# Performance work log

Measured on AMD Instinct MI355X. Metric: run time of the kernel, lower is better.

Reference implementation:

```python
import jax, jax.numpy as jnp
import numpy as np

B, T, N, F, E, L = 2, 2, 10000, 128, 160000, 2


def setup_inputs() -> dict:
    key = jax.random.key(0)
    k = jax.random.split(key, 6)
    feature = jax.random.normal(k[0], (B, T, N, F), jnp.float32)
    edge_src = jax.random.randint(k[1], (E,), 0, N, jnp.int32)
    edge_dst = jax.random.randint(k[2], (E,), 0, N, jnp.int32)
    s = 1.0 / np.sqrt(F).astype(np.float32)
    W_self = jax.random.normal(k[3], (L, F, F), jnp.float32) * s
    W_neigh = jax.random.normal(k[4], (L, F, F), jnp.float32) * s
    b = jnp.zeros((L, F), jnp.float32)
    return dict(feature=feature, W_self=W_self, W_neigh=W_neigh, b=b,
                edge_src=edge_src, edge_dst=edge_dst)


def reference(feature, W_self, W_neigh, b, edge_src, edge_dst):
    # feature: [B, T, N, Fin]; edge (src -> dst) as in dgl.from_scipy(csr).
    Bs, Ts, Ns, Fin = feature.shape
    num_layers = W_self.shape[0]
    # in-degree per dst node; mean over zero in-degree nodes is 0 (DGL semantics)
    deg = jax.ops.segment_sum(jnp.ones(edge_dst.shape, jnp.float32), edge_dst,
                              num_segments=Ns)
    inv_deg = jnp.where(deg > 0, 1.0 / jnp.maximum(deg, 1.0), 0.0)  # [N]
    # node-major layout for gather/scatter: [N, B, T, F]
    h = jnp.transpose(feature, (2, 0, 1, 3))
    for l in range(num_layers):
        msg = h[edge_src]  # [E, B, T, F] irregular gather
        agg = jax.ops.segment_sum(msg, edge_dst, num_segments=Ns)
        h_neigh = agg * inv_deg[:, None, None, None]  # mean aggregation
        h = (jnp.einsum('nbtf,fg->nbtg', h, W_self[l])
             + jnp.einsum('nbtf,fg->nbtg', h_neigh, W_neigh[l])
             + b[l])
    # res.permute(0,2,1,3) in torch -> [B, T, N, Fout]
    return jnp.transpose(h, (1, 2, 0, 3))
```

## Files before the change

### kernel.cpp

```cpp
#include <hip/hip_runtime.h>

constexpr int N_  = 10000;
constexpr int F_  = 128;
constexpr int E_  = 160000;
constexpr int BT_ = 4;
constexpr int M_  = N_ * BT_;
constexpr int CAP = 64;

typedef __attribute__((ext_vector_type(8))) short bf16x8;
typedef __attribute__((ext_vector_type(4))) float f32x4;
typedef __attribute__((ext_vector_type(2))) float f32x2;
typedef __attribute__((ext_vector_type(8))) unsigned short u16x8;

static __device__ inline float bf2f(unsigned short u) {
    union { unsigned int i; float f; } v; v.i = ((unsigned int)u) << 16; return v.f;
}
static __device__ inline unsigned short f2bf(float f) {
    union { float f; unsigned int i; } v; v.f = f;
    unsigned int x = v.i;
    return (unsigned short)((x + 0x7fffu + ((x >> 16) & 1u)) >> 16);
}


__global__ __launch_bounds__(256) void k_pre(const float4* __restrict__ feat,
        unsigned short* __restrict__ h0, unsigned char* __restrict__ h8,
        const int* __restrict__ src, const int* __restrict__ dst,
        int* __restrict__ cursor, int* __restrict__ bucket,
        const float* __restrict__ Wself, const float* __restrict__ Wneigh,
        unsigned short* __restrict__ Wp) {
    const int b = blockIdx.x;
    const int tid = threadIdx.x;
    if (b < 625) {
        int e = b * 256 + tid;
        int d = dst[e];
        int p = atomicAdd(&cursor[d], 1);
        if (p < CAP) bucket[d * CAP + p] = src[e];
    } else if (b < 657) {
        int t = (b - 625) * 256 + tid;
        int mat = t >> 11;
        int r = t & 2047;
        int kb = r >> 9;
        int nb = (r >> 6) & 7;
        int lane = r & 63;
        int l = mat >> 1, s = mat & 1;
        const float* W = (s ? Wneigh : Wself) + (size_t)l * F_ * F_;
        int k0 = kb * 32 + (lane >> 4) * 8;
        int n  = nb * 16 + (lane & 15);
        unsigned short* dstp = Wp + (size_t)mat * 16384 +
                               (size_t)((kb * 8 + nb) * 64 + lane) * 8;
#pragma unroll
        for (int j = 0; j < 8; j++) dstp[j] = f2bf(W[(size_t)(k0 + j) * F_ + n]);
    } else {
        int i = (b - 657) * 256 + tid;
        int f4 = i & 31;
        int m  = i >> 5;
        int n  = m >> 2;
        int bt = m & 3;
        float4 v = feat[(bt * N_ + n) * 32 + f4];
        ushort4 o;
        o.x = f2bf(v.x); o.y = f2bf(v.y); o.z = f2bf(v.z); o.w = f2bf(v.w);
        *(ushort4*)(h0 + (size_t)m * 128 + f4 * 4) = o;
        int w0 = __builtin_amdgcn_cvt_pk_fp8_f32(v.x, v.y, 0, false);
        int w1 = __builtin_amdgcn_cvt_pk_fp8_f32(v.z, v.w, w0, true);
        *(unsigned int*)(h8 + (size_t)m * 128 + f4 * 4) = (unsigned int)w1;
    }
}


template <bool LAST>
__global__ __launch_bounds__(128) void k_fused(const unsigned short* __restrict__ h,
        const unsigned char* __restrict__ g8, unsigned char* __restrict__ s8out,
        const int* __restrict__ cursor, const int* __restrict__ bucket,
        const unsigned short* __restrict__ Wp, const float* __restrict__ bias,
        void* __restrict__ outv) {
    __shared__ unsigned short aggs[2][4][4][136];
    const int tid  = threadIdx.x;
    const int wave = tid >> 6, lane = tid & 63;
    const int m0   = blockIdx.x * 32 + wave * 16;
    const int node0 = m0 >> 2;
    const int col  = lane & 15;
    const int quad = lane >> 4;

#pragma unroll
    for (int nl = 0; nl < 4; nl++) {
        const int n = node0 + nl;
        const int deg = cursor[n];
        const int nn = deg < CAP ? deg : CAP;
        float acc[8] = {0, 0, 0, 0, 0, 0, 0, 0};
        int idx = bucket[n * CAP + (lane < nn ? lane : 0)];
#pragma unroll 8
        for (int e = 0; e < nn; e++) {
            int s = __builtin_amdgcn_readlane(idx, e);
            uint2 a8 = *(const uint2*)(g8 + (size_t)s * 512 + lane * 8);
            f32x2 p0 = __builtin_amdgcn_cvt_pk_f32_fp8(a8.x, false);
            f32x2 p1 = __builtin_amdgcn_cvt_pk_f32_fp8(a8.x, true);
            f32x2 p2 = __builtin_amdgcn_cvt_pk_f32_fp8(a8.y, false);
            f32x2 p3 = __builtin_amdgcn_cvt_pk_f32_fp8(a8.y, true);
            acc[0] += p0.x; acc[1] += p0.y; acc[2] += p1.x; acc[3] += p1.y;
            acc[4] += p2.x; acc[5] += p2.y; acc[6] += p3.x; acc[7] += p3.y;
        }
        float w = (deg > 0) ? 1.0f / (float)deg : 0.0f;
        u16x8 o;
#pragma unroll
        for (int j = 0; j < 8; j++) o[j] = f2bf(acc[j] * w);
        *(u16x8*)&aggs[wave][nl][lane >> 4][(lane & 15) * 8] = o;
    }

    f32x4 acc[8];
#pragma unroll
    for (int nb = 0; nb < 8; nb++) {
        float b = bias[nb * 16 + col];
        acc[nb] = (f32x4){b, b, b, b};
    }

    const unsigned short* A0 = h + (size_t)(m0 + col) * 128 + quad * 8;
    const unsigned short* As = &aggs[wave][col >> 2][col & 3][quad * 8];
    const unsigned short* B0 = Wp + (size_t)lane * 8;
    const unsigned short* B1 = B0 + 16384;

#pragma unroll
    for (int kb = 0; kb < 4; kb++) {
        bf16x8 a = *(const bf16x8*)(A0 + kb * 32);
#pragma unroll
        for (int nb = 0; nb < 8; nb++) {
            bf16x8 b = *(const bf16x8*)(B0 + (size_t)((kb * 8 + nb) * 64) * 8);
            acc[nb] = __builtin_amdgcn_mfma_f32_16x16x32_bf16(a, b, acc[nb], 0, 0, 0);
        }
    }
#pragma unroll
    for (int kb = 0; kb < 4; kb++) {
        bf16x8 a = *(const bf16x8*)(As + kb * 32);
#pragma unroll
        for (int nb = 0; nb < 8; nb++) {
            bf16x8 b = *(const bf16x8*)(B1 + (size_t)((kb * 8 + nb) * 64) * 8);
            acc[nb] = __builtin_amdgcn_mfma_f32_16x16x32_bf16(a, b, acc[nb], 0, 0, 0);
        }
    }

    if (LAST) {
        float* out = (float*)outv;
#pragma unroll
        for (int nb = 0; nb < 8; nb++) {
#pragma unroll
            for (int r = 0; r < 4; r++) {
                int m = m0 + quad * 4 + r;
                int node = m >> 2, bt = m & 3;
                out[((size_t)bt * N_ + node) * 128 + nb * 16 + col] = acc[nb][r];
            }
        }
    } else {
        unsigned short* out = (unsigned short*)outv;
#pragma unroll
        for (int nb = 0; nb < 8; nb++) {
#pragma unroll
            for (int r = 0; r < 4; r++) {
                int m = m0 + quad * 4 + r;
                out[(size_t)m * 128 + nb * 16 + col] = f2bf(acc[nb][r]);
                int p = __builtin_amdgcn_cvt_pk_fp8_f32(acc[nb][r], acc[nb][r],
                                                        0, false);
                s8out[(size_t)m * 128 + nb * 16 + col] = (unsigned char)(p & 0xff);
            }
        }
    }
}


extern "C" void kernel_launch(void* const* d_in, const int* in_sizes, int n_in,
                              void* d_out, int out_size, void* d_ws, size_t ws_size,
                              hipStream_t stream) {
    const float* feature = (const float*)d_in[0];
    const float* W_self  = (const float*)d_in[1];
    const float* W_neigh = (const float*)d_in[2];
    const float* bias    = (const float*)d_in[3];
    const int*   e_src   = (const int*)d_in[4];
    const int*   e_dst   = (const int*)d_in[5];
    float*       out     = (float*)d_out;

    char* ws = (char*)d_ws;
    unsigned short* h0   = (unsigned short*)ws;  ws += (size_t)M_ * F_ * 2;
    unsigned short* h1   = (unsigned short*)ws;  ws += (size_t)M_ * F_ * 2;
    unsigned char*  h08  = (unsigned char*)ws;   ws += (size_t)M_ * F_;
    unsigned char*  h18  = (unsigned char*)ws;   ws += (size_t)M_ * F_;
    unsigned short* Wp   = (unsigned short*)ws;  ws += (size_t)4 * 16384 * 2;
    int*   cursor  = (int*)ws;                   ws += (size_t)N_ * 4;
    int*   bucket  = (int*)ws;                   ws += (size_t)N_ * CAP * 4;

    hipMemsetAsync(cursor, 0, (size_t)N_ * 4, stream);

    k_pre<<<5657, 256, 0, stream>>>((const float4*)feature, h0, h08, e_src,
                                    e_dst, cursor, bucket, W_self, W_neigh, Wp);

    const int gb = M_ / 32;
    k_fused<false><<<gb, 128, 0, stream>>>(h0, h08, h18, cursor, bucket, Wp,
                                           bias, h1);
    k_fused<true><<<gb, 128, 0, stream>>>(h1, h18, nullptr, cursor, bucket,
                                          Wp + 2 * 16384, bias + F_, out);
}
```

Before: 165.5 us.

## Split fused layer work so each wave gathers one node and computes two column tiles

Each block now covers 16 rows (4 nodes) with 4 waves instead of 32 rows with 2 waves. Each wave gathers the neighbours of a single node, the waves sync through shared memory, and each wave then computes 2 of the 8 output column tiles. This spreads the serial per-node gather over more waves and gives more parallelism and occupancy. The gather loop is rounded up to a multiple of 8 by pointing padding edges at a zero sentinel row added to the fp8 buffers and zeroed in the preprocessing kernel. The self-feature A tile is loaded before the gather so its latency overlaps it. The cost is a block-level barrier, and the A operand and weight fragments are now reloaded by more blocks.

```diff
diff --git a/kernel.cpp b/kernel.cpp
--- a/kernel.cpp
+++ b/kernel.cpp
@@ -12,9 +12,6 @@
 typedef __attribute__((ext_vector_type(2))) float f32x2;
 typedef __attribute__((ext_vector_type(8))) unsigned short u16x8;
 
-static __device__ inline float bf2f(unsigned short u) {
-    union { unsigned int i; float f; } v; v.i = ((unsigned int)u) << 16; return v.f;
-}
 static __device__ inline unsigned short f2bf(float f) {
     union { float f; unsigned int i; } v; v.f = f;
     unsigned int x = v.i;
@@ -24,6 +21,7 @@
 
 __global__ __launch_bounds__(256) void k_pre(const float4* __restrict__ feat,
         unsigned short* __restrict__ h0, unsigned char* __restrict__ h8,
+        unsigned char* __restrict__ h18z,
         const int* __restrict__ src, const int* __restrict__ dst,
         int* __restrict__ cursor, int* __restrict__ bucket,
         const float* __restrict__ Wself, const float* __restrict__ Wneigh,
@@ -36,6 +34,15 @@
         int p = atomicAdd(&cursor[d], 1);
         if (p < CAP) bucket[d * CAP + p] = src[e];
     } else if (b < 657) {
+        if (b == 625) {
+            if (tid < 64) {
+                uint2 z; z.x = 0u; z.y = 0u;
+                *(uint2*)(h8 + (size_t)N_ * 512 + tid * 8) = z;
+            } else if (tid < 128) {
+                uint2 z; z.x = 0u; z.y = 0u;
+                *(uint2*)(h18z + (size_t)N_ * 512 + (tid - 64) * 8) = z;
+            }
+        }
         int t = (b - 625) * 256 + tid;
         int mat = t >> 11;
         int r = t & 2047;
@@ -68,95 +75,111 @@
 
 
 template <bool LAST>
-__global__ __launch_bounds__(128) void k_fused(const unsigned short* __restrict__ h,
+__global__ __launch_bounds__(256) void k_fused(const unsigned short* __restrict__ h,
         const unsigned char* __restrict__ g8, unsigned char* __restrict__ s8out,
         const int* __restrict__ cursor, const int* __restrict__ bucket,
         const unsigned short* __restrict__ Wp, const float* __restrict__ bias,
         void* __restrict__ outv) {
-    __shared__ unsigned short aggs[2][4][4][136];
+    __shared__ unsigned short aggs[4][4][136];
     const int tid  = threadIdx.x;
     const int wave = tid >> 6, lane = tid & 63;
-    const int m0   = blockIdx.x * 32 + wave * 16;
+    const int m0   = blockIdx.x * 16;
     const int node0 = m0 >> 2;
     const int col  = lane & 15;
     const int quad = lane >> 4;
 
-#pragma unroll
-    for (int nl = 0; nl < 4; nl++) {
-        const int n = node0 + nl;
-        const int deg = cursor[n];
-        const int nn = deg < CAP ? deg : CAP;
-        float acc[8] = {0, 0, 0, 0, 0, 0, 0, 0};
-        int idx = bucket[n * CAP + (lane < nn ? lane : 0)];
-#pragma unroll 8
-        for (int e = 0; e < nn; e++) {
-            int s = __builtin_amdgcn_readlane(idx, e);
+    const unsigned short* A0 = h + (size_t)(m0 + col) * 128 + quad * 8;
+    bf16x8 aA[4];
+#pragma unroll
+    for (int kb = 0; kb < 4; kb++) aA[kb] = *(const bf16x8*)(A0 + kb * 32);
+
+    const int n   = node0 + wave;
+    const int deg = cursor[n];
+    const int nn  = deg < CAP ? deg : CAP;
+    const int nn8 = (nn + 7) & ~7;
+    int idx = bucket[n * CAP + (lane < nn ? lane : 0)];
+
+    float acc8[8] = {0.f, 0.f, 0.f, 0.f, 0.f, 0.f, 0.f, 0.f};
+    for (int e0 = 0; e0 < nn8; e0 += 8) {
+#pragma unroll
+        for (int u = 0; u < 8; u++) {
+            int e = e0 + u;
+            int s = (e < nn) ? __builtin_amdgcn_readlane(idx, e) : N_;
             uint2 a8 = *(const uint2*)(g8 + (size_t)s * 512 + lane * 8);
             f32x2 p0 = __builtin_amdgcn_cvt_pk_f32_fp8(a8.x, false);
             f32x2 p1 = __builtin_amdgcn_cvt_pk_f32_fp8(a8.x, true);
             f32x2 p2 = __builtin_amdgcn_cvt_pk_f32_fp8(a8.y, false);
             f32x2 p3 = __builtin_amdgcn_cvt_pk_f32_fp8(a8.y, true);
-            acc[0] += p0.x; acc[1] += p0.y; acc[2] += p1.x; acc[3] += p1.y;
-            acc[4] += p2.x; acc[5] += p2.y; acc[6] += p3.x; acc[7] += p3.y;
-        }
+            acc8[0] += p0.x; acc8[1] += p0.y;
+            acc8[2] += p1.x; acc8[3] += p1.y;
+            acc8[4] += p2.x; acc8[5] += p2.y;
+            acc8[6] += p3.x; acc8[7] += p3.y;
+        }
+    }
+    {
         float w = (deg > 0) ? 1.0f / (float)deg : 0.0f;
         u16x8 o;
 #pragma unroll
-        for (int j = 0; j < 8; j++) o[j] = f2bf(acc[j] * w);
-        *(u16x8*)&aggs[wave][nl][lane >> 4][(lane & 15) * 8] = o;
-    }
-
-    f32x4 acc[8];
-#pragma unroll
-    for (int nb = 0; nb < 8; nb++) {
-        float b = bias[nb * 16 + col];
-        acc[nb] = (f32x4){b, b, b, b};
-    }
-
-    const unsigned short* A0 = h + (size_t)(m0 + col) * 128 + quad * 8;
-    const unsigned short* As = &aggs[wave][col >> 2][col & 3][quad * 8];
+        for (int j = 0; j < 8; j++) o[j] = f2bf(acc8[j] * w);
+        *(u16x8*)&aggs[wave][lane >> 4][(lane & 15) * 8] = o;
+    }
+    __syncthreads();
+
+    const int np = wave;
+    f32x4 acc[2];
+#pragma unroll
+    for (int j = 0; j < 2; j++) {
+        float b = bias[(np * 2 + j) * 16 + col];
+        acc[j] = (f32x4){b, b, b, b};
+    }
+
+    const unsigned short* As = &aggs[col >> 2][col & 3][quad * 8];
     const unsigned short* B0 = Wp + (size_t)lane * 8;
     const unsigned short* B1 = B0 + 16384;
 
 #pragma unroll
     for (int kb = 0; kb < 4; kb++) {
-        bf16x8 a = *(const bf16x8*)(A0 + kb * 32);
-#pragma unroll
-        for (int nb = 0; nb < 8; nb++) {
+        bf16x8 a = aA[kb];
+#pragma unroll
+        for (int j = 0; j < 2; j++) {
+            int nb = np * 2 + j;
             bf16x8 b = *(const bf16x8*)(B0 + (size_t)((kb * 8 + nb) * 64) * 8);
-            acc[nb] = __builtin_amdgcn_mfma_f32_16x16x32_bf16(a, b, acc[nb], 0, 0, 0);
+            acc[j] = __builtin_amdgcn_mfma_f32_16x16x32_bf16(a, b, acc[j], 0, 0, 0);
         }
     }
 #pragma unroll
     for (int kb = 0; kb < 4; kb++) {
         bf16x8 a = *(const bf16x8*)(As + kb * 32);
 #pragma unroll
-        for (int nb = 0; nb < 8; nb++) {
+        for (int j = 0; j < 2; j++) {
+            int nb = np * 2 + j;
             bf16x8 b = *(const bf16x8*)(B1 + (size_t)((kb * 8 + nb) * 64) * 8);
-            acc[nb] = __builtin_amdgcn_mfma_f32_16x16x32_bf16(a, b, acc[nb], 0, 0, 0);
+            acc[j] = __builtin_amdgcn_mfma_f32_16x16x32_bf16(a, b, acc[j], 0, 0, 0);
         }
     }
 
     if (LAST) {
         float* out = (float*)outv;
 #pragma unroll
-        for (int nb = 0; nb < 8; nb++) {
+        for (int j = 0; j < 2; j++) {
+            int nb = np * 2 + j;
 #pragma unroll
             for (int r = 0; r < 4; r++) {
                 int m = m0 + quad * 4 + r;
                 int node = m >> 2, bt = m & 3;
-                out[((size_t)bt * N_ + node) * 128 + nb * 16 + col] = acc[nb][r];
+                out[((size_t)bt * N_ + node) * 128 + nb * 16 + col] = acc[j][r];
             }
         }
     } else {
         unsigned short* out = (unsigned short*)outv;
 #pragma unroll
-        for (int nb = 0; nb < 8; nb++) {
+        for (int j = 0; j < 2; j++) {
+            int nb = np * 2 + j;
 #pragma unroll
             for (int r = 0; r < 4; r++) {
                 int m = m0 + quad * 4 + r;
-                out[(size_t)m * 128 + nb * 16 + col] = f2bf(acc[nb][r]);
-                int p = __builtin_amdgcn_cvt_pk_fp8_f32(acc[nb][r], acc[nb][r],
+                out[(size_t)m * 128 + nb * 16 + col] = f2bf(acc[j][r]);
+                int p = __builtin_amdgcn_cvt_pk_fp8_f32(acc[j][r], acc[j][r],
                                                         0, false);
                 s8out[(size_t)m * 128 + nb * 16 + col] = (unsigned char)(p & 0xff);
             }
@@ -179,20 +202,20 @@
     char* ws = (char*)d_ws;
     unsigned short* h0   = (unsigned short*)ws;  ws += (size_t)M_ * F_ * 2;
     unsigned short* h1   = (unsigned short*)ws;  ws += (size_t)M_ * F_ * 2;
-    unsigned char*  h08  = (unsigned char*)ws;   ws += (size_t)M_ * F_;
-    unsigned char*  h18  = (unsigned char*)ws;   ws += (size_t)M_ * F_;
+    unsigned char*  h08  = (unsigned char*)ws;   ws += (size_t)M_ * F_ + 512;
+    unsigned char*  h18  = (unsigned char*)ws;   ws += (size_t)M_ * F_ + 512;
     unsigned short* Wp   = (unsigned short*)ws;  ws += (size_t)4 * 16384 * 2;
     int*   cursor  = (int*)ws;                   ws += (size_t)N_ * 4;
     int*   bucket  = (int*)ws;                   ws += (size_t)N_ * CAP * 4;
 
     hipMemsetAsync(cursor, 0, (size_t)N_ * 4, stream);
 
-    k_pre<<<5657, 256, 0, stream>>>((const float4*)feature, h0, h08, e_src,
+    k_pre<<<5657, 256, 0, stream>>>((const float4*)feature, h0, h08, h18, e_src,
                                     e_dst, cursor, bucket, W_self, W_neigh, Wp);
 
-    const int gb = M_ / 32;
-    k_fused<false><<<gb, 128, 0, stream>>>(h0, h08, h18, cursor, bucket, Wp,
+    const int gb = M_ / 16;
+    k_fused<false><<<gb, 256, 0, stream>>>(h0, h08, h18, cursor, bucket, Wp,
                                            bias, h1);
-    k_fused<true><<<gb, 128, 0, stream>>>(h1, h18, nullptr, cursor, bucket,
+    k_fused<true><<<gb, 256, 0, stream>>>(h1, h18, nullptr, cursor, bucket,
                                           Wp + 2 * 16384, bias + F_, out);
 }
```

Result: faster. 139.8 us (-15.5%).
